# Kernel optimization log

Hardware: AMD Instinct MI355X
Metric: run time of the kernel (lower is better)

## Reference

```python
import jax, jax.numpy as jnp
import numpy as np

N = 50000          # num nodes
E = 800000         # num edges (before self loops)
F_IN = 128         # input node features
HID = 64           # hidden_dim from source
HEADS = 4
NUM_CLASSES = 5
NEG_SLOPE = 0.2    # PyG GATConv default negative_slope


def setup_inputs() -> dict:
    key = jax.random.key(0)
    ks = jax.random.split(key, 14)
    def gl(k, shape, fan):
        return jax.random.normal(k, shape, jnp.float32) * (1.0 / np.sqrt(fan))
    x = jax.random.normal(ks[0], (N, F_IN), jnp.float32)
    edge_index = jax.random.randint(ks[1], (2, E), 0, N, dtype=jnp.int32)
    # layer 1: in=128, heads=4, out=64, concat
    W1 = gl(ks[2], (F_IN, HEADS * HID), F_IN)
    a_src1 = gl(ks[3], (HEADS, HID), HID)
    a_dst1 = gl(ks[4], (HEADS, HID), HID)
    b1 = jax.random.normal(ks[5], (HEADS * HID,), jnp.float32) * 0.01
    # layer 2: in=256, heads=4, out=64, concat
    W2 = gl(ks[6], (HEADS * HID, HEADS * HID), HEADS * HID)
    a_src2 = gl(ks[7], (HEADS, HID), HID)
    a_dst2 = gl(ks[8], (HEADS, HID), HID)
    b2 = jax.random.normal(ks[9], (HEADS * HID,), jnp.float32) * 0.01
    # layer 3: in=256, heads=1, out=5, concat (heads=1)
    W3 = gl(ks[10], (HEADS * HID, 1 * NUM_CLASSES), HEADS * HID)
    a_src3 = gl(ks[11], (1, NUM_CLASSES), NUM_CLASSES)
    a_dst3 = gl(ks[12], (1, NUM_CLASSES), NUM_CLASSES)
    b3 = jax.random.normal(ks[13], (NUM_CLASSES,), jnp.float32) * 0.01
    return {"x": x, "edge_index": edge_index,
            "W1": W1, "a_src1": a_src1, "a_dst1": a_dst1, "b1": b1,
            "W2": W2, "a_src2": a_src2, "a_dst2": a_dst2, "b2": b2,
            "W3": W3, "a_src3": a_src3, "a_dst3": a_dst3, "b3": b3}


def gat_conv(x, src, dst, W, a_src, a_dst, b, heads, out_ch):
    """PyG-style GATConv (concat=True, eval mode, self-loops already in src/dst)."""
    n = x.shape[0]
    h = (x @ W).reshape(n, heads, out_ch)              # [N,H,C]
    al_s = jnp.sum(h * a_src, axis=-1)                 # [N,H]
    al_d = jnp.sum(h * a_dst, axis=-1)                 # [N,H]
    # per-edge unnormalized attention
    e = jax.nn.leaky_relu(al_s[src] + al_d[dst], NEG_SLOPE)   # [E,H]
    # segment softmax over incoming edges of each destination node
    m = jax.ops.segment_max(e, dst, num_segments=n)    # [N,H]
    e = jnp.exp(e - m[dst])
    s = jax.ops.segment_sum(e, dst, num_segments=n)    # [N,H]
    alpha = e / (s[dst] + 1e-16)                       # [E,H]
    # gather-weight-scatter aggregation
    out = jax.ops.segment_sum(h[src] * alpha[..., None], dst, num_segments=n)  # [N,H,C]
    return out.reshape(n, heads * out_ch) + b


def reference(x, edge_index, W1, a_src1, a_dst1, b1, W2, a_src2, a_dst2, b2,
              W3, a_src3, a_dst3, b3):
    n = x.shape[0]
    # PyG GATConv adds self-loops by default
    loops = jnp.arange(n, dtype=edge_index.dtype)
    src = jnp.concatenate([edge_index[0], loops])
    dst = jnp.concatenate([edge_index[1], loops])
    h = jax.nn.relu(gat_conv(x, src, dst, W1, a_src1, a_dst1, b1, HEADS, HID))
    h = jax.nn.relu(gat_conv(h, src, dst, W2, a_src2, a_dst2, b2, HEADS, HID))
    out = gat_conv(h, src, dst, W3, a_src3, a_dst3, b3, 1, NUM_CLASSES)
    return out
```

## Files before the change

kernel.cpp:

```cpp
#include <hip/hip_runtime.h>
#include <hip/hip_bf16.h>
#include <cstddef>


typedef _Float16 h4 __attribute__((ext_vector_type(4)));
typedef _Float16 f16x4 __attribute__((ext_vector_type(4)));
typedef _Float16 f16x8 __attribute__((ext_vector_type(8)));
typedef float f32x4 __attribute__((ext_vector_type(4)));

#define ECAP 96
#define LSTR 40


__global__ void zero_i32(int* __restrict__ p, int n) {
  int i = blockIdx.x * 256 + threadIdx.x;
  if (i < n) p[i] = 0;
}

__global__ void edge_histogram(const int* __restrict__ ei, int E, int nnodes,
                               int* __restrict__ counts) {
  int e = blockIdx.x * 256 + threadIdx.x;
  int tot = E + nnodes;
  if (e >= tot) return;
  int dst = (e < E) ? ei[E + e] : (e - E);
  atomicAdd(&counts[dst], 1);
}

__global__ void scan_block(const int* __restrict__ in, int* __restrict__ out,
                           int* __restrict__ sums, int n) {
  __shared__ int tmp[256];
  int i = blockIdx.x * 256 + threadIdx.x;
  int v = (i < n) ? in[i] : 0;
  tmp[threadIdx.x] = v;
  __syncthreads();
  for (int off = 1; off < 256; off <<= 1) {
    int t = (threadIdx.x >= off) ? tmp[threadIdx.x - off] : 0;
    __syncthreads();
    tmp[threadIdx.x] += t;
    __syncthreads();
  }
  if (i < n) out[i] = tmp[threadIdx.x] - v;
  if (sums && threadIdx.x == 255) sums[blockIdx.x] = tmp[255];
}

__global__ void add_offsets(int* __restrict__ row_ptr, const int* __restrict__ offs,
                            int* __restrict__ nextp, int n, int total) {
  int i = blockIdx.x * 256 + threadIdx.x;
  if (i < n) {
    int v = row_ptr[i] + offs[blockIdx.x];
    row_ptr[i] = v;
    nextp[i] = v;
  }
  if (i == 0) row_ptr[n] = total;
}

__global__ void edge_scatter(const int* __restrict__ ei, int E, int nnodes,
                             int* __restrict__ nextp, int* __restrict__ col_idx) {
  int e = blockIdx.x * 256 + threadIdx.x;
  int tot = E + nnodes;
  if (e >= tot) return;
  int src = (e < E) ? ei[e] : (e - E);
  int dst = (e < E) ? ei[E + e] : (e - E);
  int pos = atomicAdd(&nextp[dst], 1);
  col_idx[pos] = src;
}


__global__ __launch_bounds__(256) void gemm_al(
    const float* __restrict__ A, const float* __restrict__ B,
    _Float16* __restrict__ C16, const float* __restrict__ a_src,
    const float* __restrict__ a_dst, float* __restrict__ alS,
    float* __restrict__ alD, int M, int K) {
  __shared__ _Float16 As16[128][LSTR];
  __shared__ _Float16 Bs16[128][LSTR];
  int t = threadIdx.x;
  int m0 = blockIdx.x * 128;
  int by = blockIdx.y;
  int n0 = by * 128;

  int l = t & 63;
  int w = t >> 6;
  int wr = w >> 1, wc = w & 1;
  int lr = l & 15;
  int lk = (l >> 4) * 8;

  int colB = t & 127;
  int kqB = t >> 7;

  f32x4 acc[4][4];
#pragma unroll
  for (int i = 0; i < 4; ++i)
#pragma unroll
    for (int j = 0; j < 4; ++j) acc[i][j] = (f32x4){0.f, 0.f, 0.f, 0.f};

  const float4 f40 = {0.f, 0.f, 0.f, 0.f};
  for (int k0 = 0; k0 < K; k0 += 32) {
#pragma unroll
    for (int r = 0; r < 4; ++r) {
      int idx = t + r * 256;
      int row = idx >> 3;
      int q = idx & 7;
      int gr = m0 + row;
      float4 v = (gr < M) ? *(const float4*)&A[(size_t)gr * K + k0 + q * 4]
                          : f40;
      f16x4 hv = {(_Float16)v.x, (_Float16)v.y, (_Float16)v.z, (_Float16)v.w};
      *(f16x4*)&As16[row][q * 4] = hv;
    }
#pragma unroll
    for (int half = 0; half < 2; ++half) {
      f16x8 hv;
#pragma unroll
      for (int j = 0; j < 8; ++j) {
        int k = kqB * 16 + half * 8 + j;
        hv[j] = (_Float16)B[(size_t)(k0 + k) * 256 + n0 + colB];
      }
      *(f16x8*)&Bs16[colB][kqB * 16 + half * 8] = hv;
    }
    __syncthreads();
    f16x8 af0 = *(const f16x8*)&As16[wr * 64 + 0 * 16 + lr][lk];
    f16x8 af1 = *(const f16x8*)&As16[wr * 64 + 1 * 16 + lr][lk];
    f16x8 af2 = *(const f16x8*)&As16[wr * 64 + 2 * 16 + lr][lk];
    f16x8 af3 = *(const f16x8*)&As16[wr * 64 + 3 * 16 + lr][lk];
#pragma unroll
    for (int j = 0; j < 4; ++j) {
      f16x8 bf = *(const f16x8*)&Bs16[wc * 64 + j * 16 + lr][lk];
      acc[0][j] = __builtin_amdgcn_mfma_f32_16x16x32_f16(af0, bf, acc[0][j], 0, 0, 0);
      acc[1][j] = __builtin_amdgcn_mfma_f32_16x16x32_f16(af1, bf, acc[1][j], 0, 0, 0);
      acc[2][j] = __builtin_amdgcn_mfma_f32_16x16x32_f16(af2, bf, acc[2][j], 0, 0, 0);
      acc[3][j] = __builtin_amdgcn_mfma_f32_16x16x32_f16(af3, bf, acc[3][j], 0, 0, 0);
    }
    __syncthreads();
  }

  int head = by * 2 + wc;
  float as4[4], ad4[4];
#pragma unroll
  for (int j = 0; j < 4; ++j) {
    as4[j] = a_src[head * 64 + j * 16 + lr];
    ad4[j] = a_dst[head * 64 + j * 16 + lr];
  }
#pragma unroll
  for (int i = 0; i < 4; ++i) {
#pragma unroll
    for (int reg = 0; reg < 4; ++reg) {
      int gr = m0 + wr * 64 + i * 16 + (l >> 4) * 4 + reg;
      float ps = acc[i][0][reg] * as4[0] + acc[i][1][reg] * as4[1] +
                 acc[i][2][reg] * as4[2] + acc[i][3][reg] * as4[3];
      float pd = acc[i][0][reg] * ad4[0] + acc[i][1][reg] * ad4[1] +
                 acc[i][2][reg] * ad4[2] + acc[i][3][reg] * ad4[3];
#pragma unroll
      for (int off = 1; off < 16; off <<= 1) {
        ps += __shfl_xor(ps, off);
        pd += __shfl_xor(pd, off);
      }
      if (gr < M) {
#pragma unroll
        for (int j = 0; j < 4; ++j)
          C16[(size_t)gr * 256 + n0 + wc * 64 + j * 16 + lr] =
              (_Float16)acc[i][j][reg];
        if (lr == 0) {
          alS[gr * 4 + head] = ps;
          alD[gr * 4 + head] = pd;
        }
      }
    }
  }
}


template <bool RELU>
__global__ __launch_bounds__(256) void gat_aggregate(
    const _Float16* __restrict__ h, const float* __restrict__ al_s,
    const float* __restrict__ al_d, const int* __restrict__ row_ptr,
    const int* __restrict__ col_idx, const float* __restrict__ bias,
    float* __restrict__ out, int nnodes) {
  __shared__ float e_lds[4][ECAP * 4];
  int wv = threadIdx.x >> 6;
  int n = blockIdx.x * 4 + wv;
  if (n >= nnodes) return;
  int l = threadIdx.x & 63;
  int hd = l >> 4;
  int sub = l & 15;
  int beg = row_ptr[n], end = row_ptr[n + 1];
  int deg = end - beg;
  float ad = al_d[n * 4 + hd];

  float m = -3.0e38f;
  for (int j0 = 0; j0 < deg; j0 += 16) {
    int j = j0 + sub;
    float e = -3.0e38f;
    if (j < deg) {
      int src = col_idx[beg + j];
      e = al_s[src * 4 + hd] + ad;
      e = fmaxf(e, 0.2f * e);
      if (j < ECAP) e_lds[wv][j * 4 + hd] = e;
    }
    m = fmaxf(m, e);
  }
#pragma unroll
  for (int off = 1; off < 16; off <<= 1) m = fmaxf(m, __shfl_xor(m, off));
  __syncthreads();

  float s = 0.f;
  float4 acc = {0.f, 0.f, 0.f, 0.f};
  int jcap = deg < ECAP ? deg : ECAP;
  int j = 0;
  for (; j + 8 <= jcap; j += 8) {
    int si[8];
    h4 hv[8];
    float p[8];
#pragma unroll
    for (int u = 0; u < 8; ++u) si[u] = col_idx[beg + j + u];
#pragma unroll
    for (int u = 0; u < 8; ++u)
      hv[u] = *(const h4*)&h[(size_t)si[u] * 256 + l * 4];
#pragma unroll
    for (int u = 0; u < 8; ++u) p[u] = __expf(e_lds[wv][(j + u) * 4 + hd] - m);
#pragma unroll
    for (int u = 0; u < 8; ++u) {
      s += p[u];
      acc.x += p[u] * (float)hv[u][0];
      acc.y += p[u] * (float)hv[u][1];
      acc.z += p[u] * (float)hv[u][2];
      acc.w += p[u] * (float)hv[u][3];
    }
  }
  for (; j < deg; ++j) {
    int src = col_idx[beg + j];
    float e;
    if (j < ECAP) {
      e = e_lds[wv][j * 4 + hd];
    } else {
      e = al_s[src * 4 + hd] + ad;
      e = fmaxf(e, 0.2f * e);
    }
    float p = __expf(e - m);
    s += p;
    h4 hv = *(const h4*)&h[(size_t)src * 256 + l * 4];
    acc.x += p * (float)hv[0];
    acc.y += p * (float)hv[1];
    acc.z += p * (float)hv[2];
    acc.w += p * (float)hv[3];
  }
  float inv = 1.f / (s + 1e-16f);
  float4 bv = *(const float4*)&bias[l * 4];
  float4 o = {acc.x * inv + bv.x, acc.y * inv + bv.y, acc.z * inv + bv.z,
              acc.w * inv + bv.w};
  if (RELU) {
    o.x = fmaxf(o.x, 0.f);
    o.y = fmaxf(o.y, 0.f);
    o.z = fmaxf(o.z, 0.f);
    o.w = fmaxf(o.w, 0.f);
  }
  *(float4*)&out[(size_t)n * 256 + l * 4] = o;
}


__global__ __launch_bounds__(256) void gemm3_al(const float* __restrict__ Hin,
                                                const float* __restrict__ W3,
                                                const float* __restrict__ a_src3,
                                                const float* __restrict__ a_dst3,
                                                float* __restrict__ h3,
                                                float* __restrict__ al_s,
                                                float* __restrict__ al_d,
                                                int nnodes) {
  int n = blockIdx.x * 4 + (threadIdx.x >> 6);
  if (n >= nnodes) return;
  int l = threadIdx.x & 63;
  float4 hv = *(const float4*)&Hin[(size_t)n * 256 + l * 4];
  float acc[5];
#pragma unroll
  for (int cc = 0; cc < 5; ++cc) {
    acc[cc] = hv.x * W3[(l * 4 + 0) * 5 + cc] + hv.y * W3[(l * 4 + 1) * 5 + cc] +
              hv.z * W3[(l * 4 + 2) * 5 + cc] + hv.w * W3[(l * 4 + 3) * 5 + cc];
  }
#pragma unroll
  for (int cc = 0; cc < 5; ++cc)
#pragma unroll
    for (int off = 32; off; off >>= 1) acc[cc] += __shfl_xor(acc[cc], off);
  if (l == 0) {
    float as = 0.f, adv = 0.f;
#pragma unroll
    for (int cc = 0; cc < 5; ++cc) {
      h3[(size_t)n * 5 + cc] = acc[cc];
      as += acc[cc] * a_src3[cc];
      adv += acc[cc] * a_dst3[cc];
    }
    al_s[n] = as;
    al_d[n] = adv;
  }
}


__global__ __launch_bounds__(256) void gat_aggregate3(
    const float* __restrict__ h3, const float* __restrict__ al_s,
    const float* __restrict__ al_d, const int* __restrict__ row_ptr,
    const int* __restrict__ col_idx, const float* __restrict__ b3,
    float* __restrict__ out, int nnodes) {
  __shared__ float e_lds[4][ECAP];
  int wv = threadIdx.x >> 6;
  int n = blockIdx.x * 4 + wv;
  if (n >= nnodes) return;
  int l = threadIdx.x & 63;
  int beg = row_ptr[n], end = row_ptr[n + 1];
  int deg = end - beg;
  float ad = al_d[n];

  float m = -3.0e38f;
  for (int j0 = 0; j0 < deg; j0 += 64) {
    int j = j0 + l;
    float e = -3.0e38f;
    if (j < deg) {
      int src = col_idx[beg + j];
      e = al_s[src] + ad;
      e = fmaxf(e, 0.2f * e);
      if (j < ECAP) e_lds[wv][j] = e;
    }
    m = fmaxf(m, e);
  }
#pragma unroll
  for (int off = 1; off < 64; off <<= 1) m = fmaxf(m, __shfl_xor(m, off));

  float sp = 0.f;
  for (int j = l; j < deg; j += 64) {
    float e;
    if (j < ECAP) {
      e = e_lds[wv][j];
    } else {
      int src = col_idx[beg + j];
      e = al_s[src] + ad;
      e = fmaxf(e, 0.2f * e);
    }
    sp += __expf(e - m);
  }
#pragma unroll
  for (int off = 1; off < 64; off <<= 1) sp += __shfl_xor(sp, off);
  float s = sp;

  float acc = 0.f;
  if (l < 5) {
    for (int j = 0; j < deg; ++j) {
      float e;
      if (j < ECAP) {
        e = e_lds[wv][j];
      } else {
        int src0 = col_idx[beg + j];
        e = al_s[src0] + ad;
        e = fmaxf(e, 0.2f * e);
      }
      float p = __expf(e - m);
      int src = col_idx[beg + j];
      acc += p * h3[(size_t)src * 5 + l];
    }
    out[(size_t)n * 5 + l] = acc / (s + 1e-16f) + b3[l];
  }
}


extern "C" void kernel_launch(void* const* d_in, const int* in_sizes, int n_in,
                              void* d_out, int out_size, void* d_ws, size_t ws_size,
                              hipStream_t stream) {
  const float* x = (const float*)d_in[0];
  const int* ei = (const int*)d_in[1];
  const float* W1 = (const float*)d_in[2];
  const float* as1 = (const float*)d_in[3];
  const float* ad1 = (const float*)d_in[4];
  const float* b1 = (const float*)d_in[5];
  const float* W2 = (const float*)d_in[6];
  const float* as2 = (const float*)d_in[7];
  const float* ad2 = (const float*)d_in[8];
  const float* b2 = (const float*)d_in[9];
  const float* W3 = (const float*)d_in[10];
  const float* as3 = (const float*)d_in[11];
  const float* ad3 = (const float*)d_in[12];
  const float* b3 = (const float*)d_in[13];

  int N = in_sizes[0] / 128;
  int E = in_sizes[1] / 2;
  int tot = E + N;

  char* w = (char*)d_ws;
  size_t off = 0;
  auto alloc = [&](size_t bytes) -> void* {
    void* p = w + off;
    off += (bytes + 255) & ~(size_t)255;
    return p;
  };
  _Float16* h16 = (_Float16*)alloc((size_t)N * 256 * 2);
  float* bufB = (float*)alloc((size_t)N * 256 * 4);
  float* bufC = (float*)alloc((size_t)N * 256 * 4);
  float* h3 = (float*)alloc((size_t)N * 5 * 4);
  float* alS = (float*)alloc((size_t)N * 4 * 4);
  float* alD = (float*)alloc((size_t)N * 4 * 4);
  int* row_ptr = (int*)alloc(((size_t)N + 1) * 4);
  int* nextp = (int*)alloc((size_t)N * 4);
  int* bsums = (int*)alloc(256 * 4);
  int* col_idx = (int*)alloc((size_t)tot * 4);
  (void)ws_size;

  int nbN = (N + 255) / 256;
  int nbE = (tot + 255) / 256;
  int nb4 = (N + 3) / 4;

  zero_i32<<<nbN, 256, 0, stream>>>(nextp, N);
  edge_histogram<<<nbE, 256, 0, stream>>>(ei, E, N, nextp);
  scan_block<<<nbN, 256, 0, stream>>>(nextp, row_ptr, bsums, N);
  scan_block<<<1, 256, 0, stream>>>(bsums, bsums, nullptr, nbN);
  add_offsets<<<nbN, 256, 0, stream>>>(row_ptr, bsums, nextp, N, tot);
  edge_scatter<<<nbE, 256, 0, stream>>>(ei, E, N, nextp, col_idx);

  dim3 g1((N + 127) / 128, 2);

  gemm_al<<<g1, 256, 0, stream>>>(x, W1, h16, as1, ad1, alS, alD, N, 128);
  gat_aggregate<true><<<nb4, 256, 0, stream>>>(h16, alS, alD, row_ptr, col_idx,
                                               b1, bufB, N);
  gemm_al<<<g1, 256, 0, stream>>>(bufB, W2, h16, as2, ad2, alS, alD, N, 256);
  gat_aggregate<true><<<nb4, 256, 0, stream>>>(h16, alS, alD, row_ptr, col_idx,
                                               b2, bufC, N);
  gemm3_al<<<nb4, 256, 0, stream>>>(bufC, W3, as3, ad3, h3, alS, alD, N);
  gat_aggregate3<<<nb4, 256, 0, stream>>>(h3, alS, alD, row_ptr, col_idx, b3,
                                          (float*)d_out, N);
}
```

Baseline: 477.4 us.

## Store layer-1 output in fp16 and widen aggregation gathers to 16-byte loads

The aggregation kernel now has each half-wave handle alternate edges, and each lane gathers 8 fp16 features (16 bytes) per edge instead of 4. The two halves' partial sums are then combined with a cross-half shuffle. Layer-1 output is written as fp16, and the second GEMM reads it directly without a float-to-half conversion, cutting intermediate write and read traffic in half. The costs are extra shuffles for the reduction, an exp computed per half-wave, and fp16 rounding of the activation, which the GEMM already applied before.

```diff
diff --git a/kernel.cpp b/kernel.cpp
--- a/kernel.cpp
+++ b/kernel.cpp
@@ -66,8 +66,9 @@
 }
 
 
+template <typename AT>
 __global__ __launch_bounds__(256) void gemm_al(
-    const float* __restrict__ A, const float* __restrict__ B,
+    const AT* __restrict__ A, const float* __restrict__ B,
     _Float16* __restrict__ C16, const float* __restrict__ a_src,
     const float* __restrict__ a_dst, float* __restrict__ alS,
     float* __restrict__ alD, int M, int K) {
@@ -95,16 +96,31 @@
 
   const float4 f40 = {0.f, 0.f, 0.f, 0.f};
   for (int k0 = 0; k0 < K; k0 += 32) {
-#pragma unroll
-    for (int r = 0; r < 4; ++r) {
-      int idx = t + r * 256;
-      int row = idx >> 3;
-      int q = idx & 7;
-      int gr = m0 + row;
-      float4 v = (gr < M) ? *(const float4*)&A[(size_t)gr * K + k0 + q * 4]
-                          : f40;
-      f16x4 hv = {(_Float16)v.x, (_Float16)v.y, (_Float16)v.z, (_Float16)v.w};
-      *(f16x4*)&As16[row][q * 4] = hv;
+    if constexpr (sizeof(AT) == 4) {
+#pragma unroll
+      for (int r = 0; r < 4; ++r) {
+        int idx = t + r * 256;
+        int row = idx >> 3;
+        int q = idx & 7;
+        int gr = m0 + row;
+        float4 v = (gr < M) ? *(const float4*)&A[(size_t)gr * K + k0 + q * 4]
+                            : f40;
+        f16x4 hv = {(_Float16)v.x, (_Float16)v.y, (_Float16)v.z,
+                    (_Float16)v.w};
+        *(f16x4*)&As16[row][q * 4] = hv;
+      }
+    } else {
+#pragma unroll
+      for (int r = 0; r < 2; ++r) {
+        int idx = t + r * 256;
+        int row = idx >> 2;
+        int q = idx & 3;
+        int gr = m0 + row;
+        f16x8 hv = (f16x8){0, 0, 0, 0, 0, 0, 0, 0};
+        if (gr < M)
+          hv = *(const f16x8*)&A[(size_t)gr * K + k0 + q * 8];
+        *(f16x8*)&As16[row][q * 8] = hv;
+      }
     }
 #pragma unroll
     for (int half = 0; half < 2; ++half) {
@@ -168,13 +184,14 @@
 }
 
 
-template <bool RELU>
+template <bool RELU, typename OT>
 __global__ __launch_bounds__(256) void gat_aggregate(
     const _Float16* __restrict__ h, const float* __restrict__ al_s,
     const float* __restrict__ al_d, const int* __restrict__ row_ptr,
     const int* __restrict__ col_idx, const float* __restrict__ bias,
-    float* __restrict__ out, int nnodes) {
+    OT* __restrict__ out, int nnodes) {
   __shared__ float e_lds[4][ECAP * 4];
+  __shared__ float m_lds[4][4];
   int wv = threadIdx.x >> 6;
   int n = blockIdx.x * 4 + wv;
   if (n >= nnodes) return;
@@ -199,60 +216,91 @@
   }
 #pragma unroll
   for (int off = 1; off < 16; off <<= 1) m = fmaxf(m, __shfl_xor(m, off));
+  if (sub == 0) m_lds[wv][hd] = m;
   __syncthreads();
 
+  int half = l >> 5;
+  int lr = l & 31;
+  int hh = lr >> 3;
+  float mh = m_lds[wv][hh];
+  float adh = al_d[n * 4 + hh];
   float s = 0.f;
-  float4 acc = {0.f, 0.f, 0.f, 0.f};
+  float acc[8];
+#pragma unroll
+  for (int q = 0; q < 8; ++q) acc[q] = 0.f;
+
   int jcap = deg < ECAP ? deg : ECAP;
   int j = 0;
   for (; j + 8 <= jcap; j += 8) {
-    int si[8];
-    h4 hv[8];
-    float p[8];
-#pragma unroll
-    for (int u = 0; u < 8; ++u) si[u] = col_idx[beg + j + u];
-#pragma unroll
-    for (int u = 0; u < 8; ++u)
-      hv[u] = *(const h4*)&h[(size_t)si[u] * 256 + l * 4];
-#pragma unroll
-    for (int u = 0; u < 8; ++u) p[u] = __expf(e_lds[wv][(j + u) * 4 + hd] - m);
-#pragma unroll
-    for (int u = 0; u < 8; ++u) {
-      s += p[u];
-      acc.x += p[u] * (float)hv[u][0];
-      acc.y += p[u] * (float)hv[u][1];
-      acc.z += p[u] * (float)hv[u][2];
-      acc.w += p[u] * (float)hv[u][3];
-    }
-  }
-  for (; j < deg; ++j) {
-    int src = col_idx[beg + j];
-    float e;
-    if (j < ECAP) {
-      e = e_lds[wv][j * 4 + hd];
-    } else {
-      e = al_s[src * 4 + hd] + ad;
-      e = fmaxf(e, 0.2f * e);
-    }
-    float p = __expf(e - m);
+    int e0 = j + 0 + half, e1 = j + 2 + half, e2 = j + 4 + half,
+        e3 = j + 6 + half;
+    int s0 = col_idx[beg + e0];
+    int s1 = col_idx[beg + e1];
+    int s2 = col_idx[beg + e2];
+    int s3 = col_idx[beg + e3];
+    f16x8 hv0 = *(const f16x8*)&h[(size_t)s0 * 256 + lr * 8];
+    f16x8 hv1 = *(const f16x8*)&h[(size_t)s1 * 256 + lr * 8];
+    f16x8 hv2 = *(const f16x8*)&h[(size_t)s2 * 256 + lr * 8];
+    f16x8 hv3 = *(const f16x8*)&h[(size_t)s3 * 256 + lr * 8];
+    float p0 = __expf(e_lds[wv][e0 * 4 + hh] - mh);
+    float p1 = __expf(e_lds[wv][e1 * 4 + hh] - mh);
+    float p2 = __expf(e_lds[wv][e2 * 4 + hh] - mh);
+    float p3 = __expf(e_lds[wv][e3 * 4 + hh] - mh);
+    s += (p0 + p1) + (p2 + p3);
+#pragma unroll
+    for (int q = 0; q < 8; ++q)
+      acc[q] += p0 * (float)hv0[q] + p1 * (float)hv1[q] +
+                p2 * (float)hv2[q] + p3 * (float)hv3[q];
+  }
+  for (; j < deg; j += 2) {
+    int ee = j + half;
+    float p = 0.f;
+    f16x8 hv = (f16x8){0, 0, 0, 0, 0, 0, 0, 0};
+    if (ee < deg) {
+      int src = col_idx[beg + ee];
+      hv = *(const f16x8*)&h[(size_t)src * 256 + lr * 8];
+      float e;
+      if (ee < ECAP) {
+        e = e_lds[wv][ee * 4 + hh];
+      } else {
+        e = al_s[src * 4 + hh] + adh;
+        e = fmaxf(e, 0.2f * e);
+      }
+      p = __expf(e - mh);
+    }
     s += p;
-    h4 hv = *(const h4*)&h[(size_t)src * 256 + l * 4];
-    acc.x += p * (float)hv[0];
-    acc.y += p * (float)hv[1];
-    acc.z += p * (float)hv[2];
-    acc.w += p * (float)hv[3];
-  }
+#pragma unroll
+    for (int q = 0; q < 8; ++q) acc[q] += p * (float)hv[q];
+  }
+
+  s += __shfl_xor(s, 32);
+#pragma unroll
+  for (int q = 0; q < 8; ++q) acc[q] += __shfl_xor(acc[q], 32);
+
   float inv = 1.f / (s + 1e-16f);
-  float4 bv = *(const float4*)&bias[l * 4];
-  float4 o = {acc.x * inv + bv.x, acc.y * inv + bv.y, acc.z * inv + bv.z,
-              acc.w * inv + bv.w};
+  int cbase = lr * 8 + half * 4;
+  float4 bv = *(const float4*)&bias[cbase];
+  float o[4];
+#pragma unroll
+  for (int q = 0; q < 4; ++q) {
+    float a = half ? acc[4 + q] : acc[q];
+    o[q] = a * inv;
+  }
+  o[0] += bv.x;
+  o[1] += bv.y;
+  o[2] += bv.z;
+  o[3] += bv.w;
   if (RELU) {
-    o.x = fmaxf(o.x, 0.f);
-    o.y = fmaxf(o.y, 0.f);
-    o.z = fmaxf(o.z, 0.f);
-    o.w = fmaxf(o.w, 0.f);
-  }
-  *(float4*)&out[(size_t)n * 256 + l * 4] = o;
+#pragma unroll
+    for (int q = 0; q < 4; ++q) o[q] = fmaxf(o[q], 0.f);
+  }
+  if constexpr (sizeof(OT) == 2) {
+    h4 ov = {(_Float16)o[0], (_Float16)o[1], (_Float16)o[2], (_Float16)o[3]};
+    *(h4*)&out[(size_t)n * 256 + cbase] = ov;
+  } else {
+    float4 ov = {o[0], o[1], o[2], o[3]};
+    *(float4*)&out[(size_t)n * 256 + cbase] = ov;
+  }
 }
 
 
@@ -387,7 +435,7 @@
     return p;
   };
   _Float16* h16 = (_Float16*)alloc((size_t)N * 256 * 2);
-  float* bufB = (float*)alloc((size_t)N * 256 * 4);
+  _Float16* bufB16 = (_Float16*)alloc((size_t)N * 256 * 2);
   float* bufC = (float*)alloc((size_t)N * 256 * 4);
   float* h3 = (float*)alloc((size_t)N * 5 * 4);
   float* alS = (float*)alloc((size_t)N * 4 * 4);
@@ -411,12 +459,13 @@
 
   dim3 g1((N + 127) / 128, 2);
 
-  gemm_al<<<g1, 256, 0, stream>>>(x, W1, h16, as1, ad1, alS, alD, N, 128);
-  gat_aggregate<true><<<nb4, 256, 0, stream>>>(h16, alS, alD, row_ptr, col_idx,
-                                               b1, bufB, N);
-  gemm_al<<<g1, 256, 0, stream>>>(bufB, W2, h16, as2, ad2, alS, alD, N, 256);
-  gat_aggregate<true><<<nb4, 256, 0, stream>>>(h16, alS, alD, row_ptr, col_idx,
-                                               b2, bufC, N);
+  gemm_al<float><<<g1, 256, 0, stream>>>(x, W1, h16, as1, ad1, alS, alD, N, 128);
+  gat_aggregate<true, _Float16><<<nb4, 256, 0, stream>>>(
+      h16, alS, alD, row_ptr, col_idx, b1, bufB16, N);
+  gemm_al<_Float16><<<g1, 256, 0, stream>>>(bufB16, W2, h16, as2, ad2, alS,
+                                            alD, N, 256);
+  gat_aggregate<true, float><<<nb4, 256, 0, stream>>>(
+      h16, alS, alD, row_ptr, col_idx, b2, bufC, N);
   gemm3_al<<<nb4, 256, 0, stream>>>(bufC, W3, as3, ad3, h3, alS, alD, N);
   gat_aggregate3<<<nb4, 256, 0, stream>>>(h3, alS, alD, row_ptr, col_idx, b3,
                                           (float*)d_out, N);
```

Result: no change. 481.8 us (+0.9%).
